# Kernel tuning notes

Hardware: AMD Instinct MI355X
Metric: run time of the kernel (lower is better)

Reference implementation:

```python
import jax, jax.numpy as jnp
import numpy as np

B, T, I, H, E = 256, 128, 512, 1024, 256


def setup_inputs() -> dict:
    key = jax.random.key(0)
    ks = jax.random.split(key, 14)
    s = lambda *d: 1.0 / np.sqrt(d[-1])
    inp = {
        "x": jax.random.normal(ks[0], (B, T, I), jnp.float32),
        # encoder LSTMCell(I, H): weights [4H, *], gate order i,f,g,o (torch)
        "enc_Wih": jax.random.uniform(ks[1], (4 * H, I), jnp.float32, -s(H), s(H)),
        "enc_Whh": jax.random.uniform(ks[2], (4 * H, H), jnp.float32, -s(H), s(H)),
        "enc_bih": jax.random.uniform(ks[3], (4 * H,), jnp.float32, -s(H), s(H)),
        "enc_bhh": jax.random.uniform(ks[4], (4 * H,), jnp.float32, -s(H), s(H)),
        # enc_fc: H -> E
        "encfc_W": jax.random.uniform(ks[5], (E, H), jnp.float32, -s(H), s(H)),
        "encfc_b": jax.random.uniform(ks[6], (E,), jnp.float32, -s(H), s(H)),
        # dec_fc: E -> H
        "decfc_W": jax.random.uniform(ks[7], (H, E), jnp.float32, -s(E), s(E)),
        "decfc_b": jax.random.uniform(ks[8], (H,), jnp.float32, -s(E), s(E)),
        # decoder LSTMCell(H + I, I)
        "dec_Wih": jax.random.uniform(ks[9], (4 * I, H + I), jnp.float32, -s(I), s(I)),
        "dec_Whh": jax.random.uniform(ks[10], (4 * I, I), jnp.float32, -s(I), s(I)),
        "dec_bih": jax.random.uniform(ks[11], (4 * I,), jnp.float32, -s(I), s(I)),
        "dec_bhh": jax.random.uniform(ks[12], (4 * I,), jnp.float32, -s(I), s(I)),
    }
    return inp


def _gates(pre):
    i, f, g, o = jnp.split(pre, 4, axis=-1)
    return jax.nn.sigmoid(i), jax.nn.sigmoid(f), jnp.tanh(g), jax.nn.sigmoid(o)


def reference(x, enc_Wih, enc_Whh, enc_bih, enc_bhh, encfc_W, encfc_b,
              decfc_W, decfc_b, dec_Wih, dec_Whh, dec_bih, dec_bhh):
    b = x.shape[0]
    # ---- encoder: precompute input projections for all timesteps ----
    x_proj = jnp.einsum('btd,gd->tbg', x, enc_Wih) + (enc_bih + enc_bhh)  # [T,B,4H]

    def enc_step(carry, xp):
        h, c = carry
        i, f, g, o = _gates(xp + h @ enc_Whh.T)
        c = f * c + i * g
        h = o * jnp.tanh(c)
        return (h, c), None

    h0 = jnp.zeros((b, H), x.dtype)
    c0 = jnp.zeros((b, H), x.dtype)
    (_, c_final), _ = jax.lax.scan(enc_step, (h0, c0), x_proj)

    # NB: original code names the returned (h, c) as (o_t_enc, h_t_enc), so
    # embd is computed from the final CELL state -- replicated faithfully.
    embd = jax.nn.relu(c_final @ encfc_W.T + encfc_b)                # [B,E]
    dec_first_hidden = jax.nn.relu(embd @ decfc_W.T + decfc_b)       # [B,H]

    # ---- decoder: input at each step is cat(dec_first_hidden, h_prev) ----
    # (eval path: teacher forcing disabled; dec states init to zeros)
    fixed = dec_first_hidden @ dec_Wih[:, :H].T + (dec_bih + dec_bhh)  # [B,4I]
    W_rec = dec_Wih[:, H:] + dec_Whh  # input second-half and hidden are both h_prev

    def dec_step(carry, _):
        h, c = carry
        i, f, g, o = _gates(fixed + h @ W_rec.T)
        c = f * c + i * g
        h = o * jnp.tanh(c)
        return (h, c), h

    hd0 = jnp.zeros((b, I), x.dtype)
    cd0 = jnp.zeros((b, I), x.dtype)
    _, hs = jax.lax.scan(dec_step, (hd0, cd0), None, length=x.shape[1])  # [T,B,I]
    outputs = jnp.transpose(hs[::-1], (1, 0, 2))  # reversed, [B,T,I]
    return outputs, embd
```

## Files before the change

### kernel.cpp

```cpp
#include <hip/hip_runtime.h>
#include <hip/hip_fp16.h>


#define B_ 256
#define T_ 128
#define I_ 512
#define H_ 1024
#define E_ 256

#define ENC_STEP 262144
#define DEC_STEP 131072
#define SENT32 0x7C7C7C7Cu

typedef _Float16 half8 __attribute__((ext_vector_type(8)));
typedef float floatx4 __attribute__((ext_vector_type(4)));

__device__ __forceinline__ float sigmoidf_(float x) { return 1.0f / (1.0f + __expf(-x)); }
__device__ __forceinline__ float tanhf_(float x) {
    x = fminf(fmaxf(x, -15.0f), 15.0f);
    float e = __expf(2.0f * x);
    return (e - 1.0f) / (e + 1.0f);
}

union HU { unsigned long long u[2]; half8 h; };

__device__ __forceinline__ void ld_chunk(const _Float16* p, HU& v) {
    const unsigned long long* q = (const unsigned long long*)p;
    v.u[0] = __hip_atomic_load(q,     __ATOMIC_RELAXED, __HIP_MEMORY_SCOPE_AGENT);
    v.u[1] = __hip_atomic_load(q + 1, __ATOMIC_RELAXED, __HIP_MEMORY_SCOPE_AGENT);
}
__device__ __forceinline__ int chunk_ok(const HU& v) {
    unsigned a = (unsigned)v.u[0], b = (unsigned)(v.u[0] >> 32);
    unsigned c = (unsigned)v.u[1], d = (unsigned)(v.u[1] >> 32);
    return (int)((a != SENT32) & (b != SENT32) & (c != SENT32) & (d != SENT32));
}
template <int STRIDE>
__device__ __forceinline__ void load_grp(const _Float16* base, HU v[4]) {
#pragma unroll
    for (int m = 0; m < 4; ++m) ld_chunk(base + (size_t)m * STRIDE, v[m]);
}
template <int STRIDE>
__device__ __forceinline__ void fix_grp(const _Float16* base, HU v[4]) {
    while (!(chunk_ok(v[0]) & chunk_ok(v[1]) & chunk_ok(v[2]) & chunk_ok(v[3]))) {
        __builtin_amdgcn_s_sleep(1);
        load_grp<STRIDE>(base, v);
    }
}

__device__ __forceinline__ half8 ldg_h8_sc1(const _Float16* p) {
    HU v; ld_chunk(p, v); return v.h;
}
__device__ __forceinline__ void stg_h2_sc1(_Float16* p, float a, float b) {
    union { _Float16 h[2]; unsigned int u; } v;
    v.h[0] = (_Float16)a; v.h[1] = (_Float16)b;
    __hip_atomic_store((unsigned int*)p, v.u, __ATOMIC_RELAXED, __HIP_MEMORY_SCOPE_AGENT);
}
__device__ __forceinline__ void wait_vm0() {
    asm volatile("s_waitcnt vmcnt(0)" ::: "memory");
}
__device__ __forceinline__ void poll_rg(int* flags, int rgbase, int lane, int target) {
    while (__hip_atomic_load(&flags[rgbase + lane], __ATOMIC_RELAXED, __HIP_MEMORY_SCOPE_AGENT) < target)
        __builtin_amdgcn_s_sleep(1);
    asm volatile("" ::: "memory");
}

__global__ void shuffle_x_kernel(const float* __restrict__ x, _Float16* __restrict__ xf) {
    const int gg   = blockIdx.x * 256 + threadIdx.x;
    const int tile = gg >> 6;
    const int lane = gg & 63;
    const int t  = tile >> 8;
    const int rt = (tile >> 4) & 15;
    const int kc = tile & 15;
    const int b  = rt * 16 + (lane & 15);
    const int j0 = kc * 32 + ((lane >> 4) << 3);
    const float* src = x + ((size_t)b * T_ + t) * I_ + j0;
    float4 f0 = *(const float4*)src;
    float4 f1 = *(const float4*)(src + 4);
    half8 h = { (_Float16)f0.x, (_Float16)f0.y, (_Float16)f0.z, (_Float16)f0.w,
                (_Float16)f1.x, (_Float16)f1.y, (_Float16)f1.z, (_Float16)f1.w };
    *(half8*)(xf + (size_t)tile * 512 + lane * 8) = h;
}

__global__ __launch_bounds__(256) void small_gemm_kernel(
    const float* __restrict__ A, int lda,
    const float* __restrict__ W, int ldw,
    const float* __restrict__ b1, const float* __restrict__ b2,
    float* __restrict__ out, int N, int K, int relu)
{
    __shared__ float sA2[32][33];
    __shared__ float sW2[32][33];
    int tid = threadIdx.x;
    int tx = tid & 15, ty = tid >> 4;
    int m0 = blockIdx.y * 32, n0 = blockIdx.x * 32;
    float acc[2][2] = {};
    for (int k0 = 0; k0 < K; k0 += 32) {
        __syncthreads();
#pragma unroll
        for (int i = 0; i < 4; ++i) {
            int e = tid + i * 256;
            int r = e >> 5, c = e & 31;
            sA2[r][c] = A[(size_t)(m0 + r) * lda + k0 + c];
            sW2[r][c] = W[(size_t)(n0 + r) * ldw + k0 + c];
        }
        __syncthreads();
#pragma unroll
        for (int k = 0; k < 32; ++k) {
            float a0 = sA2[ty * 2][k], a1 = sA2[ty * 2 + 1][k];
            float w0 = sW2[tx * 2][k], w1 = sW2[tx * 2 + 1][k];
            acc[0][0] += a0 * w0; acc[0][1] += a0 * w1;
            acc[1][0] += a1 * w0; acc[1][1] += a1 * w1;
        }
    }
#pragma unroll
    for (int i = 0; i < 2; ++i)
#pragma unroll
        for (int j = 0; j < 2; ++j) {
            int m = m0 + ty * 2 + i, n = n0 + tx * 2 + j;
            float v = acc[i][j] + b1[n] + (b2 ? b2[n] : 0.0f);
            if (relu) v = fmaxf(v, 0.0f);
            out[(size_t)m * N + n] = v;
        }
}

__global__ __launch_bounds__(256, 1) void enc_df(
    const _Float16* __restrict__ xf,
    const float* __restrict__ Wih, const float* __restrict__ Whh,
    const float* __restrict__ bih, const float* __restrict__ bhh,
    _Float16* __restrict__ hbuf, float* __restrict__ c_out)
{
    const int tid  = threadIdx.x;
    const int wave = tid >> 6, lane = tid & 63;
    const int q = lane >> 4, n15 = lane & 15;
    const int blk = blockIdx.x;
    const int rg = blk >> 6, cc = blk & 63;

    half8 bw[4][12];
#pragma unroll
    for (int g = 0; g < 4; ++g) {
        const int jc = g * H_ + cc * 16 + n15;
#pragma unroll
        for (int kc = 0; kc < 12; ++kc) {
            const int k = (4 * kc + wave) * 32 + q * 8;
            const float* src = (k < I_) ? (Wih + (size_t)jc * I_ + k)
                                        : (Whh + (size_t)jc * H_ + (k - I_));
            float4 f0 = *(const float4*)src;
            float4 f1 = *(const float4*)(src + 4);
            bw[g][kc] = half8{(_Float16)f0.x, (_Float16)f0.y, (_Float16)f0.z, (_Float16)f0.w,
                              (_Float16)f1.x, (_Float16)f1.y, (_Float16)f1.z, (_Float16)f1.w};
        }
    }

    const int hcp = tid & 7;
    const int rT  = tid >> 3;
    float breg[4][2];
#pragma unroll
    for (int g = 0; g < 4; ++g)
#pragma unroll
        for (int e = 0; e < 2; ++e) {
            const int j = g * H_ + cc * 16 + 2 * hcp + e;
            breg[g][e] = bih[j] + bhh[j];
        }
    float creg[2][2] = {{0.f, 0.f}, {0.f, 0.f}};

    __shared__ float preT[4][64][35];
    const size_t laneoff = (size_t)lane * 8;

    for (int s = 0; s < T_; ++s) {
        const _Float16* __restrict__ hcur = hbuf + (size_t)s * ENC_STEP;
        _Float16* __restrict__ hnxt = hbuf + (size_t)(s + 1) * ENC_STEP;

        floatx4 acc[4][4];
#pragma unroll
        for (int m = 0; m < 4; ++m)
#pragma unroll
            for (int n = 0; n < 4; ++n) acc[m][n] = floatx4{0.f, 0.f, 0.f, 0.f};

        half8 X[4][4];
#pragma unroll
        for (int kc = 0; kc < 4; ++kc)
#pragma unroll
            for (int m = 0; m < 4; ++m)
                X[kc][m] = *(const half8*)(xf + (((size_t)s * 16 + rg * 4 + m) * 16
                                                + (4 * kc + wave)) * 512 + laneoff);
#pragma unroll
        for (int kc = 0; kc < 4; ++kc)
#pragma unroll
            for (int n = 0; n < 4; ++n)
#pragma unroll
                for (int m = 0; m < 4; ++m)
                    acc[m][n] = __builtin_amdgcn_mfma_f32_16x16x32_f16(
                        X[kc][m], bw[n][kc], acc[m][n], 0, 0, 0);

        HU Hb[4][4];
#pragma unroll
        for (int kc = 4; kc < 8; ++kc)
            load_grp<32 * 512>(hcur + ((size_t)(rg * 4) * 32 + (4 * kc + wave - 16)) * 512
                                    + laneoff, Hb[kc - 4]);
#pragma unroll
        for (int kc = 4; kc < 12; ++kc) {
            const int sl = kc & 3;
            fix_grp<32 * 512>(hcur + ((size_t)(rg * 4) * 32 + (4 * kc + wave - 16)) * 512
                                   + laneoff, Hb[sl]);
#pragma unroll
            for (int n = 0; n < 4; ++n)
#pragma unroll
                for (int m = 0; m < 4; ++m)
                    acc[m][n] = __builtin_amdgcn_mfma_f32_16x16x32_f16(
                        Hb[sl][m].h, bw[n][kc], acc[m][n], 0, 0, 0);
            if (kc < 8)
                load_grp<32 * 512>(hcur + ((size_t)(rg * 4) * 32 + (4 * (kc + 4) + wave - 16)) * 512
                                        + laneoff, Hb[sl]);
        }

#pragma unroll
        for (int p = 0; p < 2; ++p) {
            if (p) __syncthreads();
#pragma unroll
            for (int m = 0; m < 2; ++m)
#pragma unroll
                for (int n = 0; n < 4; ++n)
#pragma unroll
                    for (int r = 0; r < 4; ++r)
                        preT[wave][n * 16 + n15][m * 16 + q * 4 + r] = acc[p * 2 + m][n][r];
            __syncthreads();
            float pg[4][2];
#pragma unroll
            for (int g = 0; g < 4; ++g)
#pragma unroll
                for (int e = 0; e < 2; ++e) {
                    const int col = g * 16 + 2 * hcp + e;
                    pg[g][e] = preT[0][col][rT] + preT[1][col][rT]
                             + preT[2][col][rT] + preT[3][col][rT] + breg[g][e];
                }
            float hv[2];
#pragma unroll
            for (int e = 0; e < 2; ++e) {
                const float ig = sigmoidf_(pg[0][e]);
                const float fg = sigmoidf_(pg[1][e]);
                const float gg = tanhf_(pg[2][e]);
                const float og = sigmoidf_(pg[3][e]);
                const float c  = fg * creg[p][e] + ig * gg;
                creg[p][e] = c;
                hv[e] = og * tanhf_(c);
            }
            const int row = p * 32 + rT;
            const int j   = cc * 16 + 2 * hcp;
            const int kch = j >> 5, j5 = j & 31;
            const int lt  = (row & 15) | ((j5 >> 3) << 4);
            stg_h2_sc1(hnxt + ((size_t)(rg * 4 + (row >> 4)) * 32 + kch) * 512
                            + lt * 8 + (j5 & 7), hv[0], hv[1]);
        }
        __syncthreads();
    }

#pragma unroll
    for (int p = 0; p < 2; ++p)
        *(float2*)(c_out + (size_t)(rg * 64 + p * 32 + rT) * H_ + cc * 16 + 2 * hcp)
            = float2{creg[p][0], creg[p][1]};
}

__global__ __launch_bounds__(256, 1) void dec_df(
    const float* __restrict__ dWih, const float* __restrict__ dWhh,
    const float* __restrict__ fixedb,
    _Float16* __restrict__ hbuf, float* __restrict__ out)
{
    const int tid  = threadIdx.x;
    const int wave = tid >> 6, lane = tid & 63;
    const int q = lane >> 4, n15 = lane & 15;
    const int blk = blockIdx.x;
    const int rg = blk >> 6, cc = blk & 63;

    half8 bw[2][4];
#pragma unroll
    for (int n = 0; n < 2; ++n) {
        const int jc = (n * 2 + (n15 >> 3)) * I_ + cc * 8 + (n15 & 7);
#pragma unroll
        for (int kc = 0; kc < 4; ++kc) {
            const int k = wave * 128 + kc * 32 + q * 8;
            const float* s0 = dWih + (size_t)jc * (H_ + I_) + H_ + k;
            const float* s1 = dWhh + (size_t)jc * I_ + k;
            float4 a0 = *(const float4*)s0, a1 = *(const float4*)(s0 + 4);
            float4 b0 = *(const float4*)s1, b1 = *(const float4*)(s1 + 4);
            bw[n][kc] = half8{(_Float16)(a0.x + b0.x), (_Float16)(a0.y + b0.y),
                              (_Float16)(a0.z + b0.z), (_Float16)(a0.w + b0.w),
                              (_Float16)(a1.x + b1.x), (_Float16)(a1.y + b1.y),
                              (_Float16)(a1.z + b1.z), (_Float16)(a1.w + b1.w)};
        }
    }

    const int hcp = tid & 3;
    const int rT  = tid >> 2;
    const int brow = rg * 64 + rT;
    float fx[4][2];
#pragma unroll
    for (int g = 0; g < 4; ++g)
#pragma unroll
        for (int e = 0; e < 2; ++e)
            fx[g][e] = fixedb[(size_t)brow * (4 * I_) + g * I_ + cc * 8 + 2 * hcp + e];
    float creg2[2] = {0.f, 0.f};

    __shared__ float preT[4][32][67];
    const size_t laneoff = (size_t)lane * 8;

    for (int s = 0; s < T_; ++s) {
        const _Float16* __restrict__ hcur = hbuf + (size_t)s * DEC_STEP;
        _Float16* __restrict__ hnxt = hbuf + (size_t)(s + 1) * DEC_STEP;

        HU Hb[4][4];
#pragma unroll
        for (int kc = 0; kc < 4; ++kc)
            load_grp<16 * 512>(hcur + ((size_t)(rg * 4) * 16 + (wave * 4 + kc)) * 512
                                    + laneoff, Hb[kc]);

        floatx4 acc[4][2];
#pragma unroll
        for (int m = 0; m < 4; ++m)
#pragma unroll
            for (int n = 0; n < 2; ++n) acc[m][n] = floatx4{0.f, 0.f, 0.f, 0.f};
#pragma unroll
        for (int kc = 0; kc < 4; ++kc) {
            fix_grp<16 * 512>(hcur + ((size_t)(rg * 4) * 16 + (wave * 4 + kc)) * 512
                                   + laneoff, Hb[kc]);
#pragma unroll
            for (int n = 0; n < 2; ++n)
#pragma unroll
                for (int m = 0; m < 4; ++m)
                    acc[m][n] = __builtin_amdgcn_mfma_f32_16x16x32_f16(
                        Hb[kc][m].h, bw[n][kc], acc[m][n], 0, 0, 0);
        }

#pragma unroll
        for (int p = 0; p < 2; ++p) {
            if (p) __syncthreads();
#pragma unroll
            for (int m = 0; m < 2; ++m)
#pragma unroll
                for (int n = 0; n < 2; ++n)
#pragma unroll
                    for (int r = 0; r < 4; ++r)
                        preT[wave][n * 16 + n15][m * 16 + q * 4 + r] = acc[p * 2 + m][n][r];
            __syncthreads();
            if ((rT >> 5) == p) {
                const int rl = rT & 31;
                float pg[4][2];
#pragma unroll
                for (int g = 0; g < 4; ++g)
#pragma unroll
                    for (int e = 0; e < 2; ++e) {
                        const int col = (g >> 1) * 16 + (g & 1) * 8 + 2 * hcp + e;
                        pg[g][e] = preT[0][col][rl] + preT[1][col][rl]
                                 + preT[2][col][rl] + preT[3][col][rl] + fx[g][e];
                    }
                float hv[2];
#pragma unroll
                for (int e = 0; e < 2; ++e) {
                    const float ig = sigmoidf_(pg[0][e]);
                    const float fg = sigmoidf_(pg[1][e]);
                    const float gg = tanhf_(pg[2][e]);
                    const float og = sigmoidf_(pg[3][e]);
                    const float c  = fg * creg2[e] + ig * gg;
                    creg2[e] = c;
                    hv[e] = og * tanhf_(c);
                }
                *(float2*)(out + ((size_t)brow * T_ + (T_ - 1 - s)) * I_ + cc * 8 + 2 * hcp)
                    = float2{hv[0], hv[1]};
                const int j = cc * 8 + 2 * hcp;
                const int kch = j >> 5, j5 = j & 31;
                const int lt  = (rT & 15) | ((j5 >> 3) << 4);
                stg_h2_sc1(hnxt + ((size_t)(rg * 4 + (rT >> 4)) * 16 + kch) * 512
                                + lt * 8 + (j5 & 7), hv[0], hv[1]);
            }
        }
        __syncthreads();
    }
}

__global__ __launch_bounds__(256, 1) void enc_persist(
    const _Float16* __restrict__ xf,
    const float* __restrict__ Wih, const float* __restrict__ Whh,
    const float* __restrict__ bih, const float* __restrict__ bhh,
    _Float16* __restrict__ hbuf, float* __restrict__ c_out, int* __restrict__ flags)
{
    const int tid  = threadIdx.x;
    const int wave = tid >> 6, lane = tid & 63;
    const int q = lane >> 4, n15 = lane & 15;
    const int blk = blockIdx.x;
    const int rg = blk >> 6, cc = blk & 63;

    half8 bw[4][12];
#pragma unroll
    for (int g = 0; g < 4; ++g) {
        const int jc = g * H_ + cc * 16 + n15;
#pragma unroll
        for (int kc = 0; kc < 12; ++kc) {
            const int k = (4 * kc + wave) * 32 + q * 8;
            const float* src = (k < I_) ? (Wih + (size_t)jc * I_ + k)
                                        : (Whh + (size_t)jc * H_ + (k - I_));
            float4 f0 = *(const float4*)src;
            float4 f1 = *(const float4*)(src + 4);
            bw[g][kc] = half8{(_Float16)f0.x, (_Float16)f0.y, (_Float16)f0.z, (_Float16)f0.w,
                              (_Float16)f1.x, (_Float16)f1.y, (_Float16)f1.z, (_Float16)f1.w};
        }
    }

    const int hcp = tid & 7;
    const int rT  = tid >> 3;
    float breg[4][2];
#pragma unroll
    for (int g = 0; g < 4; ++g)
#pragma unroll
        for (int e = 0; e < 2; ++e) {
            const int j = g * H_ + cc * 16 + 2 * hcp + e;
            breg[g][e] = bih[j] + bhh[j];
        }
    float creg[2][2] = {{0.f, 0.f}, {0.f, 0.f}};

    __shared__ float preT[4][64][35];
    const size_t laneoff = (size_t)lane * 8;

    for (int s = 0; s < T_; ++s) {
        const _Float16* __restrict__ hcur = hbuf + (size_t)(s & 1) * 262144;
        _Float16* __restrict__ hnxt = hbuf + (size_t)((s + 1) & 1) * 262144;

        floatx4 acc[4][4];
#pragma unroll
        for (int m = 0; m < 4; ++m)
#pragma unroll
            for (int n = 0; n < 4; ++n) acc[m][n] = floatx4{0.f, 0.f, 0.f, 0.f};

        half8 X[4][4];
#pragma unroll
        for (int kc = 0; kc < 4; ++kc)
#pragma unroll
            for (int m = 0; m < 4; ++m)
                X[kc][m] = *(const half8*)(xf + (((size_t)s * 16 + rg * 4 + m) * 16
                                                + (4 * kc + wave)) * 512 + laneoff);
#pragma unroll
        for (int kc = 0; kc < 4; ++kc)
#pragma unroll
            for (int n = 0; n < 4; ++n)
#pragma unroll
                for (int m = 0; m < 4; ++m)
                    acc[m][n] = __builtin_amdgcn_mfma_f32_16x16x32_f16(
                        X[kc][m], bw[n][kc], acc[m][n], 0, 0, 0);

        poll_rg(flags, rg * 64, lane, s);

        half8 Hb[4][4];
#pragma unroll
        for (int kc = 4; kc < 8; ++kc)
#pragma unroll
            for (int m = 0; m < 4; ++m)
                Hb[kc - 4][m] = ldg_h8_sc1(hcur + ((size_t)(rg * 4 + m) * 32
                                                   + (4 * kc + wave - 16)) * 512 + laneoff);
#pragma unroll
        for (int kc = 4; kc < 12; ++kc) {
            const int sl = kc & 3;
#pragma unroll
            for (int n = 0; n < 4; ++n)
#pragma unroll
                for (int m = 0; m < 4; ++m)
                    acc[m][n] = __builtin_amdgcn_mfma_f32_16x16x32_f16(
                        Hb[sl][m], bw[n][kc], acc[m][n], 0, 0, 0);
            if (kc < 8) {
#pragma unroll
                for (int m = 0; m < 4; ++m)
                    Hb[sl][m] = ldg_h8_sc1(hcur + ((size_t)(rg * 4 + m) * 32
                                                   + (4 * (kc + 4) + wave - 16)) * 512 + laneoff);
            }
        }

#pragma unroll
        for (int p = 0; p < 2; ++p) {
            if (p) __syncthreads();
#pragma unroll
            for (int m = 0; m < 2; ++m)
#pragma unroll
                for (int n = 0; n < 4; ++n)
#pragma unroll
                    for (int r = 0; r < 4; ++r)
                        preT[wave][n * 16 + n15][m * 16 + q * 4 + r] = acc[p * 2 + m][n][r];
            __syncthreads();
            float pg[4][2];
#pragma unroll
            for (int g = 0; g < 4; ++g)
#pragma unroll
                for (int e = 0; e < 2; ++e) {
                    const int col = g * 16 + 2 * hcp + e;
                    pg[g][e] = preT[0][col][rT] + preT[1][col][rT]
                             + preT[2][col][rT] + preT[3][col][rT] + breg[g][e];
                }
            float hv[2];
#pragma unroll
            for (int e = 0; e < 2; ++e) {
                const float ig = sigmoidf_(pg[0][e]);
                const float fg = sigmoidf_(pg[1][e]);
                const float gg = tanhf_(pg[2][e]);
                const float og = sigmoidf_(pg[3][e]);
                const float c  = fg * creg[p][e] + ig * gg;
                creg[p][e] = c;
                hv[e] = og * tanhf_(c);
            }
            const int row = p * 32 + rT;
            const int j   = cc * 16 + 2 * hcp;
            const int kch = j >> 5, j5 = j & 31;
            const int lt  = (row & 15) | ((j5 >> 3) << 4);
            stg_h2_sc1(hnxt + ((size_t)(rg * 4 + (row >> 4)) * 32 + kch) * 512
                            + lt * 8 + (j5 & 7), hv[0], hv[1]);
        }

        wait_vm0();
        __syncthreads();
        if (tid == 0)
            __hip_atomic_store(&flags[blk], s + 1, __ATOMIC_RELAXED, __HIP_MEMORY_SCOPE_AGENT);
    }

#pragma unroll
    for (int p = 0; p < 2; ++p)
        *(float2*)(c_out + (size_t)(rg * 64 + p * 32 + rT) * H_ + cc * 16 + 2 * hcp)
            = float2{creg[p][0], creg[p][1]};
}

__global__ __launch_bounds__(256, 1) void dec_persist(
    const float* __restrict__ dWih, const float* __restrict__ dWhh,
    const float* __restrict__ fixedb,
    _Float16* __restrict__ hbuf, float* __restrict__ out, int* __restrict__ flags)
{
    const int tid  = threadIdx.x;
    const int wave = tid >> 6, lane = tid & 63;
    const int q = lane >> 4, n15 = lane & 15;
    const int blk = blockIdx.x;
    const int rg = blk >> 6, cc = blk & 63;

    half8 bw[2][4];
#pragma unroll
    for (int n = 0; n < 2; ++n) {
        const int jc = (n * 2 + (n15 >> 3)) * I_ + cc * 8 + (n15 & 7);
#pragma unroll
        for (int kc = 0; kc < 4; ++kc) {
            const int k = wave * 128 + kc * 32 + q * 8;
            const float* s0 = dWih + (size_t)jc * (H_ + I_) + H_ + k;
            const float* s1 = dWhh + (size_t)jc * I_ + k;
            float4 a0 = *(const float4*)s0, a1 = *(const float4*)(s0 + 4);
            float4 b0 = *(const float4*)s1, b1 = *(const float4*)(s1 + 4);
            bw[n][kc] = half8{(_Float16)(a0.x + b0.x), (_Float16)(a0.y + b0.y),
                              (_Float16)(a0.z + b0.z), (_Float16)(a0.w + b0.w),
                              (_Float16)(a1.x + b1.x), (_Float16)(a1.y + b1.y),
                              (_Float16)(a1.z + b1.z), (_Float16)(a1.w + b1.w)};
        }
    }

    const int hcp = tid & 3;
    const int rT  = tid >> 2;
    const int brow = rg * 64 + rT;
    float fx[4][2];
#pragma unroll
    for (int g = 0; g < 4; ++g)
#pragma unroll
        for (int e = 0; e < 2; ++e)
            fx[g][e] = fixedb[(size_t)brow * (4 * I_) + g * I_ + cc * 8 + 2 * hcp + e];
    float creg2[2] = {0.f, 0.f};

    __shared__ float preT[4][32][67];
    const size_t laneoff = (size_t)lane * 8;

    for (int s = 0; s < T_; ++s) {
        const _Float16* __restrict__ hcur = hbuf + (size_t)(s & 1) * 131072;
        _Float16* __restrict__ hnxt = hbuf + (size_t)((s + 1) & 1) * 131072;

        poll_rg(flags, rg * 64, lane, s);

        half8 Hb[4][4];
#pragma unroll
        for (int kc = 0; kc < 4; ++kc)
#pragma unroll
            for (int m = 0; m < 4; ++m)
                Hb[kc][m] = ldg_h8_sc1(hcur + ((size_t)(rg * 4 + m) * 16
                                               + (wave * 4 + kc)) * 512 + laneoff);
        floatx4 acc[4][2];
#pragma unroll
        for (int m = 0; m < 4; ++m)
#pragma unroll
            for (int n = 0; n < 2; ++n) acc[m][n] = floatx4{0.f, 0.f, 0.f, 0.f};
#pragma unroll
        for (int kc = 0; kc < 4; ++kc)
#pragma unroll
            for (int n = 0; n < 2; ++n)
#pragma unroll
                for (int m = 0; m < 4; ++m)
                    acc[m][n] = __builtin_amdgcn_mfma_f32_16x16x32_f16(
                        Hb[kc][m], bw[n][kc], acc[m][n], 0, 0, 0);

#pragma unroll
        for (int p = 0; p < 2; ++p) {
            if (p) __syncthreads();
#pragma unroll
            for (int m = 0; m < 2; ++m)
#pragma unroll
                for (int n = 0; n < 2; ++n)
#pragma unroll
                    for (int r = 0; r < 4; ++r)
                        preT[wave][n * 16 + n15][m * 16 + q * 4 + r] = acc[p * 2 + m][n][r];
            __syncthreads();
            if ((rT >> 5) == p) {
                const int rl = rT & 31;
                float pg[4][2];
#pragma unroll
                for (int g = 0; g < 4; ++g)
#pragma unroll
                    for (int e = 0; e < 2; ++e) {
                        const int col = (g >> 1) * 16 + (g & 1) * 8 + 2 * hcp + e;
                        pg[g][e] = preT[0][col][rl] + preT[1][col][rl]
                                 + preT[2][col][rl] + preT[3][col][rl] + fx[g][e];
                    }
                float hv[2];
#pragma unroll
                for (int e = 0; e < 2; ++e) {
                    const float ig = sigmoidf_(pg[0][e]);
                    const float fg = sigmoidf_(pg[1][e]);
                    const float gg = tanhf_(pg[2][e]);
                    const float og = sigmoidf_(pg[3][e]);
                    const float c  = fg * creg2[e] + ig * gg;
                    creg2[e] = c;
                    hv[e] = og * tanhf_(c);
                }
                *(float2*)(out + ((size_t)brow * T_ + (T_ - 1 - s)) * I_ + cc * 8 + 2 * hcp)
                    = float2{hv[0], hv[1]};
                const int j = cc * 8 + 2 * hcp;
                const int kch = j >> 5, j5 = j & 31;
                const int lt  = (rT & 15) | ((j5 >> 3) << 4);
                stg_h2_sc1(hnxt + ((size_t)(rg * 4 + (rT >> 4)) * 16 + kch) * 512
                                + lt * 8 + (j5 & 7), hv[0], hv[1]);
            }
        }

        wait_vm0();
        __syncthreads();
        if (tid == 0)
            __hip_atomic_store(&flags[blk], s + 1, __ATOMIC_RELAXED, __HIP_MEMORY_SCOPE_AGENT);
    }
}

extern "C" void kernel_launch(void* const* d_in, const int* in_sizes, int n_in,
                              void* d_out_v, int out_size, void* d_ws, size_t ws_size,
                              hipStream_t stream) {
    (void)in_sizes; (void)n_in; (void)out_size;
    const float* x    = (const float*)d_in[0];
    const float* eWih = (const float*)d_in[1];
    const float* eWhh = (const float*)d_in[2];
    const float* ebih = (const float*)d_in[3];
    const float* ebhh = (const float*)d_in[4];
    const float* efcW = (const float*)d_in[5];
    const float* efcb = (const float*)d_in[6];
    const float* dfcW = (const float*)d_in[7];
    const float* dfcb = (const float*)d_in[8];
    const float* dWih = (const float*)d_in[9];
    const float* dWhh = (const float*)d_in[10];
    const float* dbih = (const float*)d_in[11];
    const float* dbhh = (const float*)d_in[12];
    float* d_out = (float*)d_out_v;

    char* ws = (char*)d_ws;
    size_t off = 0;
    auto carve = [&](size_t bytes) {
        char* p = ws + off;
        off += (bytes + 255) & ~(size_t)255;
        return p;
    };

    const size_t xf_b  = (size_t)B_ * T_ * I_ * 2;
    const size_t hbE_b = (size_t)(T_ + 1) * ENC_STEP * 2;
    const size_t hbD_b = (size_t)(T_ + 1) * DEC_STEP * 2;
    const size_t ce_b  = (size_t)B_ * H_ * 4;
    const size_t fxb_b = (size_t)B_ * 4 * I_ * 4;
    const size_t d1_b  = (size_t)B_ * H_ * 4;
    const size_t need_primary = xf_b + hbE_b + hbD_b + ce_b + fxb_b + d1_b + 4096;

    float* embd = d_out + (size_t)B_ * T_ * I_;

    if (ws_size == 0 || ws_size >= need_primary) {
        _Float16* xf     = (_Float16*)carve(xf_b);
        _Float16* hbufE  = (_Float16*)carve(hbE_b);
        _Float16* hbufD  = (_Float16*)carve(hbD_b);
        float*    c_e    = (float*)carve(ce_b);
        float*    fixedb = (float*)carve(fxb_b);
        float*    dec1   = (float*)carve(d1_b);

        hipMemsetAsync(hbufE, 0, (size_t)ENC_STEP * 2, stream);
        hipMemsetAsync((char*)hbufE + (size_t)ENC_STEP * 2, 0x7C, (size_t)T_ * ENC_STEP * 2, stream);
        hipMemsetAsync(hbufD, 0, (size_t)DEC_STEP * 2, stream);
        hipMemsetAsync((char*)hbufD + (size_t)DEC_STEP * 2, 0x7C, (size_t)T_ * DEC_STEP * 2, stream);

        shuffle_x_kernel<<<dim3(8192), 256, 0, stream>>>(x, xf);
        enc_df<<<dim3(256), 256, 0, stream>>>(xf, eWih, eWhh, ebih, ebhh, hbufE, c_e);
        small_gemm_kernel<<<dim3(E_ / 32, B_ / 32), 256, 0, stream>>>(
            c_e, H_, efcW, H_, efcb, nullptr, embd, E_, H_, 1);
        small_gemm_kernel<<<dim3(H_ / 32, B_ / 32), 256, 0, stream>>>(
            embd, E_, dfcW, E_, dfcb, nullptr, dec1, H_, E_, 1);
        small_gemm_kernel<<<dim3(4 * I_ / 32, B_ / 32), 256, 0, stream>>>(
            dec1, H_, dWih, H_ + I_, dbih, dbhh, fixedb, 4 * I_, H_, 0);
        dec_persist;
        dec_df<<<dim3(256), 256, 0, stream>>>(dWih, dWhh, fixedb, hbufD, d_out);
    } else {
        _Float16* xf     = (_Float16*)carve(xf_b);
        _Float16* hbufE  = (_Float16*)carve((size_t)2 * 262144 * 2);
        _Float16* hbufD  = (_Float16*)carve((size_t)2 * 131072 * 2);
        float*    c_e    = (float*)carve(ce_b);
        float*    fixedb = (float*)carve(fxb_b);
        float*    dec1   = (float*)carve(d1_b);
        int*      flagsE = (int*)carve(256 * 4);
        int*      flagsD = (int*)carve(256 * 4);

        hipMemsetAsync(flagsE, 0, 256 * 4, stream);
        hipMemsetAsync(flagsD, 0, 256 * 4, stream);
        hipMemsetAsync(hbufE, 0, (size_t)262144 * 2, stream);
        hipMemsetAsync(hbufD, 0, (size_t)131072 * 2, stream);

        shuffle_x_kernel<<<dim3(8192), 256, 0, stream>>>(x, xf);
        enc_persist<<<dim3(256), 256, 0, stream>>>(xf, eWih, eWhh, ebih, ebhh,
                                                   hbufE, c_e, flagsE);
        small_gemm_kernel<<<dim3(E_ / 32, B_ / 32), 256, 0, stream>>>(
            c_e, H_, efcW, H_, efcb, nullptr, embd, E_, H_, 1);
        small_gemm_kernel<<<dim3(H_ / 32, B_ / 32), 256, 0, stream>>>(
            embd, E_, dfcW, E_, dfcb, nullptr, dec1, H_, E_, 1);
        small_gemm_kernel<<<dim3(4 * I_ / 32, B_ / 32), 256, 0, stream>>>(
            dec1, H_, dWih, H_ + I_, dbih, dbhh, fixedb, 4 * I_, H_, 0);
        dec_persist<<<dim3(256), 256, 0, stream>>>(dWih, dWhh, fixedb,
                                                   hbufD, d_out, flagsD);
    }
}
```

Baseline: 1.779 ms.

## Replace encoder sentinel dataflow with flag-based persistent sync and double-buffered hidden state

The encoder used to poll sentinel values in a hidden-state buffer holding every timestep. It now uses a persistent kernel with per-block counter flags and a two-slot ping-pong buffer. Each wave bumps its block's flag with an atomic after its stores drain, and consumers poll the row group's flags before loading h. Half of the input-projection MFMAs are moved after the poll to hide polling latency. This removes the large sentinel memset and the per-element fixup checks, at the cost of flag polling and atomics on the critical path.

```diff
diff --git a/kernel.cpp b/kernel.cpp
--- a/kernel.cpp
+++ b/kernel.cpp
@@ -122,11 +122,11 @@
         }
 }
 
-__global__ __launch_bounds__(256, 1) void enc_df(
+__global__ __launch_bounds__(256, 1) void enc_persist(
     const _Float16* __restrict__ xf,
     const float* __restrict__ Wih, const float* __restrict__ Whh,
     const float* __restrict__ bih, const float* __restrict__ bhh,
-    _Float16* __restrict__ hbuf, float* __restrict__ c_out)
+    _Float16* __restrict__ hbuf, float* __restrict__ c_out, int* __restrict__ flags)
 {
     const int tid  = threadIdx.x;
     const int wave = tid >> 6, lane = tid & 63;
@@ -166,8 +166,8 @@
     const size_t laneoff = (size_t)lane * 8;
 
     for (int s = 0; s < T_; ++s) {
-        const _Float16* __restrict__ hcur = hbuf + (size_t)s * ENC_STEP;
-        _Float16* __restrict__ hnxt = hbuf + (size_t)(s + 1) * ENC_STEP;
+        const _Float16* __restrict__ hcur = hbuf + (size_t)(s & 1) * 262144;
+        _Float16* __restrict__ hnxt = hbuf + (size_t)((s + 1) & 1) * 262144;
 
         floatx4 acc[4][4];
 #pragma unroll
@@ -183,7 +183,7 @@
                 X[kc][m] = *(const half8*)(xf + (((size_t)s * 16 + rg * 4 + m) * 16
                                                 + (4 * kc + wave)) * 512 + laneoff);
 #pragma unroll
-        for (int kc = 0; kc < 4; ++kc)
+        for (int kc = 0; kc < 2; ++kc)
 #pragma unroll
             for (int n = 0; n < 4; ++n)
 #pragma unroll
@@ -191,25 +191,40 @@
                     acc[m][n] = __builtin_amdgcn_mfma_f32_16x16x32_f16(
                         X[kc][m], bw[n][kc], acc[m][n], 0, 0, 0);
 
-        HU Hb[4][4];
+        poll_rg(flags, rg * 64, lane, 4 * s);
+
+        half8 Hb[4][4];
 #pragma unroll
         for (int kc = 4; kc < 8; ++kc)
-            load_grp<32 * 512>(hcur + ((size_t)(rg * 4) * 32 + (4 * kc + wave - 16)) * 512
-                                    + laneoff, Hb[kc - 4]);
+#pragma unroll
+            for (int m = 0; m < 4; ++m)
+                Hb[kc - 4][m] = ldg_h8_sc1(hcur + ((size_t)(rg * 4 + m) * 32
+                                                   + (4 * kc + wave - 16)) * 512 + laneoff);
+
+#pragma unroll
+        for (int kc = 2; kc < 4; ++kc)
+#pragma unroll
+            for (int n = 0; n < 4; ++n)
+#pragma unroll
+                for (int m = 0; m < 4; ++m)
+                    acc[m][n] = __builtin_amdgcn_mfma_f32_16x16x32_f16(
+                        X[kc][m], bw[n][kc], acc[m][n], 0, 0, 0);
+
 #pragma unroll
         for (int kc = 4; kc < 12; ++kc) {
             const int sl = kc & 3;
-            fix_grp<32 * 512>(hcur + ((size_t)(rg * 4) * 32 + (4 * kc + wave - 16)) * 512
-                                   + laneoff, Hb[sl]);
 #pragma unroll
             for (int n = 0; n < 4; ++n)
 #pragma unroll
                 for (int m = 0; m < 4; ++m)
                     acc[m][n] = __builtin_amdgcn_mfma_f32_16x16x32_f16(
-                        Hb[sl][m].h, bw[n][kc], acc[m][n], 0, 0, 0);
-            if (kc < 8)
-                load_grp<32 * 512>(hcur + ((size_t)(rg * 4) * 32 + (4 * (kc + 4) + wave - 16)) * 512
-                                        + laneoff, Hb[sl]);
+                        Hb[sl][m], bw[n][kc], acc[m][n], 0, 0, 0);
+            if (kc < 8) {
+#pragma unroll
+                for (int m = 0; m < 4; ++m)
+                    Hb[sl][m] = ldg_h8_sc1(hcur + ((size_t)(rg * 4 + m) * 32
+                                                   + (4 * (kc + 4) + wave - 16)) * 512 + laneoff);
+            }
         }
 
 #pragma unroll
@@ -250,6 +265,10 @@
             stg_h2_sc1(hnxt + ((size_t)(rg * 4 + (row >> 4)) * 32 + kch) * 512
                             + lt * 8 + (j5 & 7), hv[0], hv[1]);
         }
+
+        wait_vm0();
+        if (lane == 0)
+            __hip_atomic_fetch_add(&flags[blk], 1, __ATOMIC_RELAXED, __HIP_MEMORY_SCOPE_AGENT);
         __syncthreads();
     }
 
@@ -373,152 +392,6 @@
         }
         __syncthreads();
     }
-}
-
-__global__ __launch_bounds__(256, 1) void enc_persist(
-    const _Float16* __restrict__ xf,
-    const float* __restrict__ Wih, const float* __restrict__ Whh,
-    const float* __restrict__ bih, const float* __restrict__ bhh,
-    _Float16* __restrict__ hbuf, float* __restrict__ c_out, int* __restrict__ flags)
-{
-    const int tid  = threadIdx.x;
-    const int wave = tid >> 6, lane = tid & 63;
-    const int q = lane >> 4, n15 = lane & 15;
-    const int blk = blockIdx.x;
-    const int rg = blk >> 6, cc = blk & 63;
-
-    half8 bw[4][12];
-#pragma unroll
-    for (int g = 0; g < 4; ++g) {
-        const int jc = g * H_ + cc * 16 + n15;
-#pragma unroll
-        for (int kc = 0; kc < 12; ++kc) {
-            const int k = (4 * kc + wave) * 32 + q * 8;
-            const float* src = (k < I_) ? (Wih + (size_t)jc * I_ + k)
-                                        : (Whh + (size_t)jc * H_ + (k - I_));
-            float4 f0 = *(const float4*)src;
-            float4 f1 = *(const float4*)(src + 4);
-            bw[g][kc] = half8{(_Float16)f0.x, (_Float16)f0.y, (_Float16)f0.z, (_Float16)f0.w,
-                              (_Float16)f1.x, (_Float16)f1.y, (_Float16)f1.z, (_Float16)f1.w};
-        }
-    }
-
-    const int hcp = tid & 7;
-    const int rT  = tid >> 3;
-    float breg[4][2];
-#pragma unroll
-    for (int g = 0; g < 4; ++g)
-#pragma unroll
-        for (int e = 0; e < 2; ++e) {
-            const int j = g * H_ + cc * 16 + 2 * hcp + e;
-            breg[g][e] = bih[j] + bhh[j];
-        }
-    float creg[2][2] = {{0.f, 0.f}, {0.f, 0.f}};
-
-    __shared__ float preT[4][64][35];
-    const size_t laneoff = (size_t)lane * 8;
-
-    for (int s = 0; s < T_; ++s) {
-        const _Float16* __restrict__ hcur = hbuf + (size_t)(s & 1) * 262144;
-        _Float16* __restrict__ hnxt = hbuf + (size_t)((s + 1) & 1) * 262144;
-
-        floatx4 acc[4][4];
-#pragma unroll
-        for (int m = 0; m < 4; ++m)
-#pragma unroll
-            for (int n = 0; n < 4; ++n) acc[m][n] = floatx4{0.f, 0.f, 0.f, 0.f};
-
-        half8 X[4][4];
-#pragma unroll
-        for (int kc = 0; kc < 4; ++kc)
-#pragma unroll
-            for (int m = 0; m < 4; ++m)
-                X[kc][m] = *(const half8*)(xf + (((size_t)s * 16 + rg * 4 + m) * 16
-                                                + (4 * kc + wave)) * 512 + laneoff);
-#pragma unroll
-        for (int kc = 0; kc < 4; ++kc)
-#pragma unroll
-            for (int n = 0; n < 4; ++n)
-#pragma unroll
-                for (int m = 0; m < 4; ++m)
-                    acc[m][n] = __builtin_amdgcn_mfma_f32_16x16x32_f16(
-                        X[kc][m], bw[n][kc], acc[m][n], 0, 0, 0);
-
-        poll_rg(flags, rg * 64, lane, s);
-
-        half8 Hb[4][4];
-#pragma unroll
-        for (int kc = 4; kc < 8; ++kc)
-#pragma unroll
-            for (int m = 0; m < 4; ++m)
-                Hb[kc - 4][m] = ldg_h8_sc1(hcur + ((size_t)(rg * 4 + m) * 32
-                                                   + (4 * kc + wave - 16)) * 512 + laneoff);
-#pragma unroll
-        for (int kc = 4; kc < 12; ++kc) {
-            const int sl = kc & 3;
-#pragma unroll
-            for (int n = 0; n < 4; ++n)
-#pragma unroll
-                for (int m = 0; m < 4; ++m)
-                    acc[m][n] = __builtin_amdgcn_mfma_f32_16x16x32_f16(
-                        Hb[sl][m], bw[n][kc], acc[m][n], 0, 0, 0);
-            if (kc < 8) {
-#pragma unroll
-                for (int m = 0; m < 4; ++m)
-                    Hb[sl][m] = ldg_h8_sc1(hcur + ((size_t)(rg * 4 + m) * 32
-                                                   + (4 * (kc + 4) + wave - 16)) * 512 + laneoff);
-            }
-        }
-
-#pragma unroll
-        for (int p = 0; p < 2; ++p) {
-            if (p) __syncthreads();
-#pragma unroll
-            for (int m = 0; m < 2; ++m)
-#pragma unroll
-                for (int n = 0; n < 4; ++n)
-#pragma unroll
-                    for (int r = 0; r < 4; ++r)
-                        preT[wave][n * 16 + n15][m * 16 + q * 4 + r] = acc[p * 2 + m][n][r];
-            __syncthreads();
-            float pg[4][2];
-#pragma unroll
-            for (int g = 0; g < 4; ++g)
-#pragma unroll
-                for (int e = 0; e < 2; ++e) {
-                    const int col = g * 16 + 2 * hcp + e;
-                    pg[g][e] = preT[0][col][rT] + preT[1][col][rT]
-                             + preT[2][col][rT] + preT[3][col][rT] + breg[g][e];
-                }
-            float hv[2];
-#pragma unroll
-            for (int e = 0; e < 2; ++e) {
-                const float ig = sigmoidf_(pg[0][e]);
-                const float fg = sigmoidf_(pg[1][e]);
-                const float gg = tanhf_(pg[2][e]);
-                const float og = sigmoidf_(pg[3][e]);
-                const float c  = fg * creg[p][e] + ig * gg;
-                creg[p][e] = c;
-                hv[e] = og * tanhf_(c);
-            }
-            const int row = p * 32 + rT;
-            const int j   = cc * 16 + 2 * hcp;
-            const int kch = j >> 5, j5 = j & 31;
-            const int lt  = (row & 15) | ((j5 >> 3) << 4);
-            stg_h2_sc1(hnxt + ((size_t)(rg * 4 + (row >> 4)) * 32 + kch) * 512
-                            + lt * 8 + (j5 & 7), hv[0], hv[1]);
-        }
-
-        wait_vm0();
-        __syncthreads();
-        if (tid == 0)
-            __hip_atomic_store(&flags[blk], s + 1, __ATOMIC_RELAXED, __HIP_MEMORY_SCOPE_AGENT);
-    }
-
-#pragma unroll
-    for (int p = 0; p < 2; ++p)
-        *(float2*)(c_out + (size_t)(rg * 64 + p * 32 + rT) * H_ + cc * 16 + 2 * hcp)
-            = float2{creg[p][0], creg[p][1]};
 }
 
 __global__ __launch_bounds__(256, 1) void dec_persist(
@@ -669,12 +542,12 @@
     };
 
     const size_t xf_b  = (size_t)B_ * T_ * I_ * 2;
-    const size_t hbE_b = (size_t)(T_ + 1) * ENC_STEP * 2;
+    const size_t hbE_b = (size_t)2 * ENC_STEP * 2;
     const size_t hbD_b = (size_t)(T_ + 1) * DEC_STEP * 2;
     const size_t ce_b  = (size_t)B_ * H_ * 4;
     const size_t fxb_b = (size_t)B_ * 4 * I_ * 4;
     const size_t d1_b  = (size_t)B_ * H_ * 4;
-    const size_t need_primary = xf_b + hbE_b + hbD_b + ce_b + fxb_b + d1_b + 4096;
+    const size_t need_primary = xf_b + hbE_b + hbD_b + ce_b + fxb_b + d1_b + 8192;
 
     float* embd = d_out + (size_t)B_ * T_ * I_;
 
@@ -685,26 +558,27 @@
         float*    c_e    = (float*)carve(ce_b);
         float*    fixedb = (float*)carve(fxb_b);
         float*    dec1   = (float*)carve(d1_b);
-
+        int*      flagsE = (int*)carve(256 * 4);
+
+        hipMemsetAsync(flagsE, 0, 256 * 4, stream);
         hipMemsetAsync(hbufE, 0, (size_t)ENC_STEP * 2, stream);
-        hipMemsetAsync((char*)hbufE + (size_t)ENC_STEP * 2, 0x7C, (size_t)T_ * ENC_STEP * 2, stream);
         hipMemsetAsync(hbufD, 0, (size_t)DEC_STEP * 2, stream);
         hipMemsetAsync((char*)hbufD + (size_t)DEC_STEP * 2, 0x7C, (size_t)T_ * DEC_STEP * 2, stream);
 
         shuffle_x_kernel<<<dim3(8192), 256, 0, stream>>>(x, xf);
-        enc_df<<<dim3(256), 256, 0, stream>>>(xf, eWih, eWhh, ebih, ebhh, hbufE, c_e);
+        enc_persist<<<dim3(256), 256, 0, stream>>>(xf, eWih, eWhh, ebih, ebhh,
+                                                   hbufE, c_e, flagsE);
         small_gemm_kernel<<<dim3(E_ / 32, B_ / 32), 256, 0, stream>>>(
             c_e, H_, efcW, H_, efcb, nullptr, embd, E_, H_, 1);
         small_gemm_kernel<<<dim3(H_ / 32, B_ / 32), 256, 0, stream>>>(
             embd, E_, dfcW, E_, dfcb, nullptr, dec1, H_, E_, 1);
         small_gemm_kernel<<<dim3(4 * I_ / 32, B_ / 32), 256, 0, stream>>>(
             dec1, H_, dWih, H_ + I_, dbih, dbhh, fixedb, 4 * I_, H_, 0);
-        dec_persist;
         dec_df<<<dim3(256), 256, 0, stream>>>(dWih, dWhh, fixedb, hbufD, d_out);
     } else {
         _Float16* xf     = (_Float16*)carve(xf_b);
-        _Float16* hbufE  = (_Float16*)carve((size_t)2 * 262144 * 2);
-        _Float16* hbufD  = (_Float16*)carve((size_t)2 * 131072 * 2);
+        _Float16* hbufE  = (_Float16*)carve((size_t)2 * ENC_STEP * 2);
+        _Float16* hbufD  = (_Float16*)carve((size_t)2 * DEC_STEP * 2);
         float*    c_e    = (float*)carve(ce_b);
         float*    fixedb = (float*)carve(fxb_b);
         float*    dec1   = (float*)carve(d1_b);
@@ -713,8 +587,8 @@
 
         hipMemsetAsync(flagsE, 0, 256 * 4, stream);
         hipMemsetAsync(flagsD, 0, 256 * 4, stream);
-        hipMemsetAsync(hbufE, 0, (size_t)262144 * 2, stream);
-        hipMemsetAsync(hbufD, 0, (size_t)131072 * 2, stream);
+        hipMemsetAsync(hbufE, 0, (size_t)ENC_STEP * 2, stream);
+        hipMemsetAsync(hbufD, 0, (size_t)DEC_STEP * 2, stream);
 
         shuffle_x_kernel<<<dim3(8192), 256, 0, stream>>>(x, xf);
         enc_persist<<<dim3(256), 256, 0, stream>>>(xf, eWih, eWhh, ebih, ebhh,
```

New measurement: 1.653 ms. 7.1% less time.

## Replace encoder sentinel polling with per-wave flag counters and split input MFMAs

Applied to the files above, without the earlier changes.

The primary encoder path stops relying on sentinel-filled (0x7C) per-step h buffers and fixup reload loops. Each wave now increments a per-block flag after its h stores drain, and consumers poll the row-group flags (target 4*s) before plain vector loads of h. Half of the input-projection MFMAs are moved after the poll so they overlap the wait and the h loads. This removes the large encoder sentinel memset and the per-chunk validation branches, at the cost of an explicit flag round-trip per step. The decoder keeps sentinel validation but checks each chunk individually.

```diff
diff --git a/kernel.cpp b/kernel.cpp
--- a/kernel.cpp
+++ b/kernel.cpp
@@ -22,7 +22,7 @@
     return (e - 1.0f) / (e + 1.0f);
 }
 
-union HU { unsigned long long u[2]; half8 h; };
+union HU { unsigned long long u[2]; unsigned v[4]; half8 h; };
 
 __device__ __forceinline__ void ld_chunk(const _Float16* p, HU& v) {
     const unsigned long long* q = (const unsigned long long*)p;
@@ -30,21 +30,18 @@
     v.u[1] = __hip_atomic_load(q + 1, __ATOMIC_RELAXED, __HIP_MEMORY_SCOPE_AGENT);
 }
 __device__ __forceinline__ int chunk_ok(const HU& v) {
-    unsigned a = (unsigned)v.u[0], b = (unsigned)(v.u[0] >> 32);
-    unsigned c = (unsigned)v.u[1], d = (unsigned)(v.u[1] >> 32);
-    return (int)((a != SENT32) & (b != SENT32) & (c != SENT32) & (d != SENT32));
-}
-template <int STRIDE>
-__device__ __forceinline__ void load_grp(const _Float16* base, HU v[4]) {
-#pragma unroll
-    for (int m = 0; m < 4; ++m) ld_chunk(base + (size_t)m * STRIDE, v[m]);
-}
-template <int STRIDE>
-__device__ __forceinline__ void fix_grp(const _Float16* base, HU v[4]) {
-    while (!(chunk_ok(v[0]) & chunk_ok(v[1]) & chunk_ok(v[2]) & chunk_ok(v[3]))) {
-        __builtin_amdgcn_s_sleep(1);
-        load_grp<STRIDE>(base, v);
-    }
+    return (int)((v.v[0] != SENT32) & (v.v[1] != SENT32)
+               & (v.v[2] != SENT32) & (v.v[3] != SENT32));
+}
+__device__ __forceinline__ half8 validate_chunk(const _Float16* p, half8 opt) {
+    HU c; c.h = opt;
+    if (!chunk_ok(c)) {
+        do {
+            __builtin_amdgcn_s_sleep(1);
+            ld_chunk(p, c);
+        } while (!chunk_ok(c));
+    }
+    return c.h;
 }
 
 __device__ __forceinline__ half8 ldg_h8_sc1(const _Float16* p) {
@@ -122,11 +119,11 @@
         }
 }
 
-__global__ __launch_bounds__(256, 1) void enc_df(
+__global__ __launch_bounds__(256, 1) void enc_l2(
     const _Float16* __restrict__ xf,
     const float* __restrict__ Wih, const float* __restrict__ Whh,
     const float* __restrict__ bih, const float* __restrict__ bhh,
-    _Float16* __restrict__ hbuf, float* __restrict__ c_out)
+    _Float16* __restrict__ hbuf, float* __restrict__ c_out, int* __restrict__ flags)
 {
     const int tid  = threadIdx.x;
     const int wave = tid >> 6, lane = tid & 63;
@@ -183,7 +180,7 @@
                 X[kc][m] = *(const half8*)(xf + (((size_t)s * 16 + rg * 4 + m) * 16
                                                 + (4 * kc + wave)) * 512 + laneoff);
 #pragma unroll
-        for (int kc = 0; kc < 4; ++kc)
+        for (int kc = 0; kc < 2; ++kc)
 #pragma unroll
             for (int n = 0; n < 4; ++n)
 #pragma unroll
@@ -191,25 +188,40 @@
                     acc[m][n] = __builtin_amdgcn_mfma_f32_16x16x32_f16(
                         X[kc][m], bw[n][kc], acc[m][n], 0, 0, 0);
 
-        HU Hb[4][4];
+        poll_rg(flags, rg * 64, lane, 4 * s);
+
+        half8 Hb[4][4];
 #pragma unroll
         for (int kc = 4; kc < 8; ++kc)
-            load_grp<32 * 512>(hcur + ((size_t)(rg * 4) * 32 + (4 * kc + wave - 16)) * 512
-                                    + laneoff, Hb[kc - 4]);
+#pragma unroll
+            for (int m = 0; m < 4; ++m)
+                Hb[kc - 4][m] = *(const half8*)(hcur + ((size_t)(rg * 4 + m) * 32
+                                                   + (4 * kc + wave - 16)) * 512 + laneoff);
+
+#pragma unroll
+        for (int kc = 2; kc < 4; ++kc)
+#pragma unroll
+            for (int n = 0; n < 4; ++n)
+#pragma unroll
+                for (int m = 0; m < 4; ++m)
+                    acc[m][n] = __builtin_amdgcn_mfma_f32_16x16x32_f16(
+                        X[kc][m], bw[n][kc], acc[m][n], 0, 0, 0);
+
 #pragma unroll
         for (int kc = 4; kc < 12; ++kc) {
             const int sl = kc & 3;
-            fix_grp<32 * 512>(hcur + ((size_t)(rg * 4) * 32 + (4 * kc + wave - 16)) * 512
-                                   + laneoff, Hb[sl]);
 #pragma unroll
             for (int n = 0; n < 4; ++n)
 #pragma unroll
                 for (int m = 0; m < 4; ++m)
                     acc[m][n] = __builtin_amdgcn_mfma_f32_16x16x32_f16(
-                        Hb[sl][m].h, bw[n][kc], acc[m][n], 0, 0, 0);
-            if (kc < 8)
-                load_grp<32 * 512>(hcur + ((size_t)(rg * 4) * 32 + (4 * (kc + 4) + wave - 16)) * 512
-                                        + laneoff, Hb[sl]);
+                        Hb[sl][m], bw[n][kc], acc[m][n], 0, 0, 0);
+            if (kc < 8) {
+#pragma unroll
+                for (int m = 0; m < 4; ++m)
+                    Hb[sl][m] = *(const half8*)(hcur + ((size_t)(rg * 4 + m) * 32
+                                                   + (4 * (kc + 4) + wave - 16)) * 512 + laneoff);
+            }
         }
 
 #pragma unroll
@@ -250,6 +262,10 @@
             stg_h2_sc1(hnxt + ((size_t)(rg * 4 + (row >> 4)) * 32 + kch) * 512
                             + lt * 8 + (j5 & 7), hv[0], hv[1]);
         }
+
+        wait_vm0();
+        if (lane == 0)
+            __hip_atomic_fetch_add(&flags[blk], 1, __ATOMIC_RELAXED, __HIP_MEMORY_SCOPE_AGENT);
         __syncthreads();
     }
 
@@ -306,11 +322,13 @@
         const _Float16* __restrict__ hcur = hbuf + (size_t)s * DEC_STEP;
         _Float16* __restrict__ hnxt = hbuf + (size_t)(s + 1) * DEC_STEP;
 
-        HU Hb[4][4];
+        half8 Hc[4][4];
 #pragma unroll
         for (int kc = 0; kc < 4; ++kc)
-            load_grp<16 * 512>(hcur + ((size_t)(rg * 4) * 16 + (wave * 4 + kc)) * 512
-                                    + laneoff, Hb[kc]);
+#pragma unroll
+            for (int m = 0; m < 4; ++m)
+                Hc[kc][m] = *(const half8*)(hcur + ((size_t)(rg * 4 + m) * 16
+                                                   + (wave * 4 + kc)) * 512 + laneoff);
 
         floatx4 acc[4][2];
 #pragma unroll
@@ -319,14 +337,17 @@
             for (int n = 0; n < 2; ++n) acc[m][n] = floatx4{0.f, 0.f, 0.f, 0.f};
 #pragma unroll
         for (int kc = 0; kc < 4; ++kc) {
-            fix_grp<16 * 512>(hcur + ((size_t)(rg * 4) * 16 + (wave * 4 + kc)) * 512
-                                   + laneoff, Hb[kc]);
+#pragma unroll
+            for (int m = 0; m < 4; ++m)
+                Hc[kc][m] = validate_chunk(hcur + ((size_t)(rg * 4 + m) * 16
+                                                  + (wave * 4 + kc)) * 512 + laneoff,
+                                           Hc[kc][m]);
 #pragma unroll
             for (int n = 0; n < 2; ++n)
 #pragma unroll
                 for (int m = 0; m < 4; ++m)
                     acc[m][n] = __builtin_amdgcn_mfma_f32_16x16x32_f16(
-                        Hb[kc][m].h, bw[n][kc], acc[m][n], 0, 0, 0);
+                        Hc[kc][m], bw[n][kc], acc[m][n], 0, 0, 0);
         }
 
 #pragma unroll
@@ -375,7 +396,7 @@
     }
 }
 
-__global__ __launch_bounds__(256, 1) void enc_persist(
+__global__ __launch_bounds__(256, 1) void enc_ring(
     const _Float16* __restrict__ xf,
     const float* __restrict__ Wih, const float* __restrict__ Whh,
     const float* __restrict__ bih, const float* __restrict__ bhh,
@@ -419,8 +440,8 @@
     const size_t laneoff = (size_t)lane * 8;
 
     for (int s = 0; s < T_; ++s) {
-        const _Float16* __restrict__ hcur = hbuf + (size_t)(s & 1) * 262144;
-        _Float16* __restrict__ hnxt = hbuf + (size_t)((s + 1) & 1) * 262144;
+        const _Float16* __restrict__ hcur = hbuf + (size_t)(s & 1) * ENC_STEP;
+        _Float16* __restrict__ hnxt = hbuf + (size_t)((s + 1) & 1) * ENC_STEP;
 
         floatx4 acc[4][4];
 #pragma unroll
@@ -444,7 +465,7 @@
                     acc[m][n] = __builtin_amdgcn_mfma_f32_16x16x32_f16(
                         X[kc][m], bw[n][kc], acc[m][n], 0, 0, 0);
 
-        poll_rg(flags, rg * 64, lane, s);
+        poll_rg(flags, rg * 64, lane, 4 * s);
 
         half8 Hb[4][4];
 #pragma unroll
@@ -510,9 +531,9 @@
         }
 
         wait_vm0();
+        if (lane == 0)
+            __hip_atomic_fetch_add(&flags[blk], 1, __ATOMIC_RELAXED, __HIP_MEMORY_SCOPE_AGENT);
         __syncthreads();
-        if (tid == 0)
-            __hip_atomic_store(&flags[blk], s + 1, __ATOMIC_RELAXED, __HIP_MEMORY_SCOPE_AGENT);
     }
 
 #pragma unroll
@@ -565,8 +586,8 @@
     const size_t laneoff = (size_t)lane * 8;
 
     for (int s = 0; s < T_; ++s) {
-        const _Float16* __restrict__ hcur = hbuf + (size_t)(s & 1) * 131072;
-        _Float16* __restrict__ hnxt = hbuf + (size_t)((s + 1) & 1) * 131072;
+        const _Float16* __restrict__ hcur = hbuf + (size_t)(s & 1) * DEC_STEP;
+        _Float16* __restrict__ hnxt = hbuf + (size_t)((s + 1) & 1) * DEC_STEP;
 
         poll_rg(flags, rg * 64, lane, s);
 
@@ -674,7 +695,7 @@
     const size_t ce_b  = (size_t)B_ * H_ * 4;
     const size_t fxb_b = (size_t)B_ * 4 * I_ * 4;
     const size_t d1_b  = (size_t)B_ * H_ * 4;
-    const size_t need_primary = xf_b + hbE_b + hbD_b + ce_b + fxb_b + d1_b + 4096;
+    const size_t need_primary = xf_b + hbE_b + hbD_b + ce_b + fxb_b + d1_b + 8192;
 
     float* embd = d_out + (size_t)B_ * T_ * I_;
 
@@ -685,26 +706,27 @@
         float*    c_e    = (float*)carve(ce_b);
         float*    fixedb = (float*)carve(fxb_b);
         float*    dec1   = (float*)carve(d1_b);
-
+        int*      flagsE = (int*)carve(256 * 4);
+
+        hipMemsetAsync(flagsE, 0, 256 * 4, stream);
         hipMemsetAsync(hbufE, 0, (size_t)ENC_STEP * 2, stream);
-        hipMemsetAsync((char*)hbufE + (size_t)ENC_STEP * 2, 0x7C, (size_t)T_ * ENC_STEP * 2, stream);
         hipMemsetAsync(hbufD, 0, (size_t)DEC_STEP * 2, stream);
         hipMemsetAsync((char*)hbufD + (size_t)DEC_STEP * 2, 0x7C, (size_t)T_ * DEC_STEP * 2, stream);
 
         shuffle_x_kernel<<<dim3(8192), 256, 0, stream>>>(x, xf);
-        enc_df<<<dim3(256), 256, 0, stream>>>(xf, eWih, eWhh, ebih, ebhh, hbufE, c_e);
+        enc_l2<<<dim3(256), 256, 0, stream>>>(xf, eWih, eWhh, ebih, ebhh,
+                                              hbufE, c_e, flagsE);
         small_gemm_kernel<<<dim3(E_ / 32, B_ / 32), 256, 0, stream>>>(
             c_e, H_, efcW, H_, efcb, nullptr, embd, E_, H_, 1);
         small_gemm_kernel<<<dim3(H_ / 32, B_ / 32), 256, 0, stream>>>(
             embd, E_, dfcW, E_, dfcb, nullptr, dec1, H_, E_, 1);
         small_gemm_kernel<<<dim3(4 * I_ / 32, B_ / 32), 256, 0, stream>>>(
             dec1, H_, dWih, H_ + I_, dbih, dbhh, fixedb, 4 * I_, H_, 0);
-        dec_persist;
         dec_df<<<dim3(256), 256, 0, stream>>>(dWih, dWhh, fixedb, hbufD, d_out);
     } else {
         _Float16* xf     = (_Float16*)carve(xf_b);
-        _Float16* hbufE  = (_Float16*)carve((size_t)2 * 262144 * 2);
-        _Float16* hbufD  = (_Float16*)carve((size_t)2 * 131072 * 2);
+        _Float16* hbufE  = (_Float16*)carve((size_t)2 * ENC_STEP * 2);
+        _Float16* hbufD  = (_Float16*)carve((size_t)2 * DEC_STEP * 2);
         float*    c_e    = (float*)carve(ce_b);
         float*    fixedb = (float*)carve(fxb_b);
         float*    dec1   = (float*)carve(d1_b);
@@ -713,12 +735,12 @@
 
         hipMemsetAsync(flagsE, 0, 256 * 4, stream);
         hipMemsetAsync(flagsD, 0, 256 * 4, stream);
-        hipMemsetAsync(hbufE, 0, (size_t)262144 * 2, stream);
-        hipMemsetAsync(hbufD, 0, (size_t)131072 * 2, stream);
+        hipMemsetAsync(hbufE, 0, (size_t)ENC_STEP * 2, stream);
+        hipMemsetAsync(hbufD, 0, (size_t)DEC_STEP * 2, stream);
 
         shuffle_x_kernel<<<dim3(8192), 256, 0, stream>>>(x, xf);
-        enc_persist<<<dim3(256), 256, 0, stream>>>(xf, eWih, eWhh, ebih, ebhh,
-                                                   hbufE, c_e, flagsE);
+        enc_ring<<<dim3(256), 256, 0, stream>>>(xf, eWih, eWhh, ebih, ebhh,
+                                                hbufE, c_e, flagsE);
         small_gemm_kernel<<<dim3(E_ / 32, B_ / 32), 256, 0, stream>>>(
             c_e, H_, efcW, H_, efcb, nullptr, embd, E_, H_, 1);
         small_gemm_kernel<<<dim3(H_ / 32, B_ / 32), 256, 0, stream>>>(
```

Result: slower. 1.991 ms (+11.9%).
